# Kernel tuning notes

Hardware: AMD Instinct MI355X
Metric: run time of the kernel (lower is better)

Reference implementation:

```python
import jax, jax.numpy as jnp
import numpy as np
from jax import lax

NUM_ITER = 10
SMOOTH = 1.0
CL_WEIGHT = 0.5


def _min_pool(x, wh, ww):
    # torch: -max_pool2d(-x) pads with -inf -> min-pool with +inf boundary
    return lax.reduce_window(x, jnp.inf, lax.min,
                             (1, 1, wh, ww), (1, 1, 1, 1),
                             [(0, 0), (0, 0), (wh // 2, wh // 2), (ww // 2, ww // 2)])


def _max_pool(x, wh, ww):
    return lax.reduce_window(x, -jnp.inf, lax.max,
                             (1, 1, wh, ww), (1, 1, 1, 1),
                             [(0, 0), (0, 0), (wh // 2, wh // 2), (ww // 2, ww // 2)])


def soft_erode(img):
    return jnp.minimum(_min_pool(img, 3, 1), _min_pool(img, 1, 3))


def soft_dilate(img):
    return _max_pool(img, 3, 3)


def soft_open(img):
    return soft_dilate(soft_erode(img))


def soft_skeleton(img, num_iter=NUM_ITER):
    # img: (B,1,H,W)
    skel = jax.nn.relu(img - soft_open(img))

    def body(i, carry):
        img_e, skel = carry
        img_e = soft_erode(img_e)
        delta = jax.nn.relu(img_e - soft_open(img_e))
        skel = skel + jax.nn.relu(delta - skel * delta)
        return (img_e, skel)

    _, skel = lax.fori_loop(0, num_iter, body, (img, skel))
    return skel


def soft_dice(pred, target, smooth=SMOOTH):
    inter = jnp.sum(pred * target)
    return (2.0 * inter + smooth) / (jnp.sum(pred) + jnp.sum(target) + smooth)


def setup_inputs() -> dict:
    key = jax.random.key(0)
    k1, k2 = jax.random.split(key)
    pred = jax.random.normal(k1, (8, 1, 1024, 1024), dtype=jnp.float32)
    target = jax.random.randint(k2, (8, 1, 1024, 1024), 0, 2, dtype=jnp.int32)
    return {"pred": pred, "target": target}


def reference(pred, target):
    pred_prob = jax.nn.sigmoid(pred)          # (B,1,H,W)
    target_f = target.astype(pred_prob.dtype)

    skel_pred = soft_skeleton(pred_prob)
    skel_target = soft_skeleton(target_f)

    tprec = (jnp.sum(skel_pred * target_f) + SMOOTH) / (jnp.sum(skel_pred) + SMOOTH)
    tsens = (jnp.sum(skel_target * pred_prob) + SMOOTH) / (jnp.sum(skel_target) + SMOOTH)
    cl_dice = 2.0 * tprec * tsens / (tprec + tsens + 1e-7)

    dice = soft_dice(pred_prob, target_f)
    combined = (1.0 - CL_WEIGHT) * dice + CL_WEIGHT * cl_dice
    loss = 1.0 - combined
    return loss
```

## Files before the change

kernel.cpp:

```cpp
#include <hip/hip_runtime.h>
#include <math.h>

#define IMG  1024
#define TILE 64
#define HALO 12
#define SPP  52
#define NPRED (90*SPP)
#define SEN2 0x40004000u

typedef _Float16 h2 __attribute__((ext_vector_type(2)));
union UH { unsigned u; h2 h; };
__device__ __forceinline__ h2 u2h(unsigned u){ UH x; x.u=u; return x.h; }
__device__ __forceinline__ unsigned h2u(h2 h){ UH x; x.h=h; return x.u; }
__device__ __forceinline__ h2 pmin(h2 a, h2 b){ return __builtin_elementwise_min(a,b); }
__device__ __forceinline__ h2 pmax(h2 a, h2 b){ return __builtin_elementwise_max(a,b); }
__device__ __forceinline__ h2 funnel(h2 hi_src, h2 lo_src){
  return u2h((h2u(lo_src)>>16) | (h2u(hi_src)<<16));
}
__device__ __forceinline__ float sigmoidf(float x){ return 1.0f/(1.0f+__expf(-x)); }
__device__ __forceinline__ h2 unsent(h2 x, h2 onev, h2 zerov){
  h2 t = pmax(x-onev, zerov); return x - t - t;
}
__device__ __forceinline__ unsigned extract8(unsigned w0, unsigned w1, unsigned w2, int bp){
  unsigned long long lo = (unsigned long long)w0 | ((unsigned long long)w1<<32);
  unsigned long long hi = (unsigned long long)w1 | ((unsigned long long)w2<<32);
  unsigned a = (unsigned)(lo >> bp);
  unsigned b = (unsigned)(hi >> (bp & 31));
  return ((bp < 32) ? a : b) & 0xFFu;
}
__device__ __forceinline__ uint4 erode5(uint4 rm, uint4 rc, uint4 rn, h2 lw, h2 rv){
  h2 a0=u2h(rc.x), a1=u2h(rc.y), a2=u2h(rc.z), a3=u2h(rc.w);
  h2 v0=pmin(u2h(rm.x), u2h(rn.x));
  h2 v1=pmin(u2h(rm.y), u2h(rn.y));
  h2 v2=pmin(u2h(rm.z), u2h(rn.z));
  h2 v3=pmin(u2h(rm.w), u2h(rn.w));
  h2 f0=funnel(a0,lw), f1=funnel(a1,a0), f2=funnel(a2,a1), f3=funnel(a3,a2), f4=funnel(rv,a3);
  uint4 e;
  e.x=h2u(pmin(pmin(f0,f1),pmin(v0,a0)));
  e.y=h2u(pmin(pmin(f1,f2),pmin(v1,a1)));
  e.z=h2u(pmin(pmin(f2,f3),pmin(v2,a2)));
  e.w=h2u(pmin(pmin(f3,f4),pmin(v3,a3)));
  return e;
}

template<bool BND>
__device__ void pipeline(const float* __restrict__ pred, const int* __restrict__ targ,
                         long base, int gr0, int gc0, int tid,
                         unsigned* A, unsigned* B, unsigned* Ta, unsigned* Tb,
                         h2 val[4], h2 skel[4], unsigned &tbits, unsigned &skbits) {
  for (int i = tid; i < 104; i += 512) {
    int r = (i < 52) ? 0 : 89, c = (i < 52) ? i : i - 52;
    A[r*SPP + c] = SEN2;  B[r*SPP + c] = SEN2;
  }
  for (int i = tid; i < 704; i += 512) {
    int r = 1 + (i >> 3), w = i & 7;
    w = (w < 2) ? w : 44 + w;
    A[r*SPP + w] = SEN2;  B[r*SPP + w] = SEN2;
  }
  if (!BND) {
    #pragma unroll
    for (int k=0;k<2;++k){
      int u = tid + (k<<9);
      if (u < 968){
        int r = u/11, q = u - r*11;
        long g = base + (long)(gr0+r)*IMG + gc0 + (q<<3);
        float4 pa = *(const float4*)(pred+g);
        float4 pb = *(const float4*)(pred+g+4);
        h2 w0 = {(_Float16)sigmoidf(pa.x), (_Float16)sigmoidf(pa.y)};
        h2 w1 = {(_Float16)sigmoidf(pa.z), (_Float16)sigmoidf(pa.w)};
        h2 w2 = {(_Float16)sigmoidf(pb.x), (_Float16)sigmoidf(pb.y)};
        h2 w3 = {(_Float16)sigmoidf(pb.z), (_Float16)sigmoidf(pb.w)};
        int o = (1+r)*SPP + 2 + (q<<2);
        uint2 d0; d0.x=h2u(w0); d0.y=h2u(w1);
        uint2 d1; d1.x=h2u(w2); d1.y=h2u(w3);
        *(uint2*)&A[o]   = d0;
        *(uint2*)&A[o+2] = d1;
      }
    }
    if (tid < 264){
      int u = tid;
      int r = u/3, w = u - r*3;
      long g = base + (long)(gr0+r)*IMG + gc0 + (w<<5);
      unsigned bits = 0;
      #pragma unroll
      for (int i=0;i<8;++i){
        if (w < 2 || i < 6) {
          int4 tv = *(const int4*)(targ + g + (i<<2));
          unsigned nib = (unsigned)(tv.x!=0) | ((unsigned)(tv.y!=0)<<1)
                       | ((unsigned)(tv.z!=0)<<2) | ((unsigned)(tv.w!=0)<<3);
          bits |= nib << (i<<2);
        }
      }
      if (w==2) bits |= 0xFF000000u;
      Ta[u] = bits;
    }
  } else {
    for (int i=tid; i<88*44; i+=512){
      int r = i/44, wd = i - r*44;
      int gr = gr0 + r;
      bool rok = (unsigned)gr < (unsigned)IMG;
      int gca = gc0 + (wd<<1), gcb = gca + 1;
      _Float16 va = (_Float16)2.0f, vb = (_Float16)2.0f;
      if (rok && (unsigned)gca < (unsigned)IMG) va = (_Float16)sigmoidf(pred[base + (long)gr*IMG + gca]);
      if (rok && (unsigned)gcb < (unsigned)IMG) vb = (_Float16)sigmoidf(pred[base + (long)gr*IMG + gcb]);
      h2 w; w.x = va; w.y = vb;
      A[(1+r)*SPP + 2 + wd] = h2u(w);
    }
    for (int u=tid; u<264; u+=512){
      int r = u/3, w = u - r*3;
      int gr = gr0 + r;
      bool rok = (unsigned)gr < (unsigned)IMG;
      unsigned bits = 0;
      for (int b=0;b<32;++b){
        int c = (w<<5) + b;
        unsigned bit = 1;
        if (c < 88) {
          int gc = gc0 + c;
          if (rok && (unsigned)gc < (unsigned)IMG) bit = (unsigned)(targ[base+(long)gr*IMG+gc] != 0);
        }
        bits |= bit << b;
      }
      Ta[u] = bits;
    }
  }
  __syncthreads();

  unsigned cm0=~0u, cm1=~0u, cm2=0x00FFFFFFu;
  bool colO = false;
  if (BND) {
    int lo = (-gc0 > 0) ? -gc0 : 0;
    int hi = (IMG - gc0 < 88) ? (IMG - gc0) : 88;
    colO = (lo > 0) || (hi < 88);
    unsigned m[3];
    #pragma unroll
    for (int w=0; w<3; ++w){
      int l = lo - (w<<5); if (l<0) l=0;
      int h = hi - (w<<5); if (h>32) h=32;
      unsigned mm = 0;
      if (h > l) {
        unsigned top = (h>=32)? ~0u : ((1u<<h)-1u);
        unsigned bot = (l<=0)? 0u : ((1u<<l)-1u);
        mm = top & ~bot;
      }
      m[w]=mm;
    }
    cm0=m[0]; cm1=m[1]; cm2=m[2] & 0x00FFFFFF;
  }

  const int es  = tid / 12,  eq  = tid - es*12;
  const int s2  = es*2;
  const int ew  = eq << 2;
  const int cl1 = (eq<<3) + 3;
  const int ch1 = (eq<<3) - 4;
  const bool has2 = (tid < 16);
  const int u2  = 512 + tid;
  const int es2 = u2/12, eq2 = u2 - es2*12;
  const int s2b = es2*2, ew2 = eq2<<2;
  const int cl2 = (eq2<<3)+3, ch2 = (eq2<<3)-4;

  const bool tex = (tid < 258);
  const int  to  = 3 + tid;
  const int  twd = tid % 3;

  const int qc = tid & 7;
  const int rg = tid >> 3;
  const int pr = HALO + rg;
  const int wq = 8 + (qc<<2);
  const int bp = 12 + (qc<<3);

  h2 ep[4];
  {
    uint4 a0 = *(const uint4*)&A[(pr+1)*SPP + wq];
    ep[0]=u2h(a0.x); ep[1]=u2h(a0.y); ep[2]=u2h(a0.z); ep[3]=u2h(a0.w);
    #pragma unroll
    for (int i=0;i<4;++i){ val[i]=ep[i]; skel[i]=(h2)(_Float16)0.0f; }
  }
  {
    int oa = pr*3;
    tbits = extract8(Ta[oa],Ta[oa+1],Ta[oa+2],bp);
  }
  unsigned tp0=0,tp1=0,tp2=0, sk0=0,sk1=0,sk2=0;
  const bool td = (tid < 64);
  const int tro = (12 + tid)*3;
  if (td) { tp0=Ta[tro]; tp1=Ta[tro+1]; tp2=Ta[tro+2]; }

  const h2 onev  = {(_Float16)1.0f,(_Float16)1.0f};
  const h2 zerov = {(_Float16)0.0f,(_Float16)0.0f};

  for (int j=0;j<11;++j){
    {
      auto ERO = [&](int s2_, int ew_){
        uint4 rm = *(const uint4*)&A[s2_*SPP + ew_];
        uint4 rc = *(const uint4*)&A[(s2_+1)*SPP + ew_];
        #pragma unroll
        for (int t=0;t<2;++t){
          uint4 rn = *(const uint4*)&A[(s2_+2+t)*SPP + ew_];
          int brc = s2_+1+t;
          h2 lw = u2h(A[brc*SPP + ew_ - 1]);
          h2 rv = u2h(A[brc*SPP + ew_ + 4]);
          *(uint4*)&B[brc*SPP + ew_] = erode5(rm, rc, rn, lw, rv);
          rm = rc; rc = rn;
        }
      };
      if ((s2+1 >= j+1) && (s2 <= 86-j) && (cl1 >= j+1) && (ch1 <= 86-j))
        ERO(s2, ew);
      if (has2 && (s2b+1 >= j+1) && (s2b <= 86-j) && (cl2 >= j+1) && (ch2 <= 86-j))
        ERO(s2b, ew2);
    }
    if (tex){
      unsigned own=Ta[to], up=Ta[to-3], dn=Ta[to+3];
      unsigned le = (twd>0)? Ta[to-1] : ~0u;
      unsigned ri = (twd<2)? Ta[to+1] : ~0u;
      unsigned h = own & ((own>>1)|(ri<<31)) & ((own<<1)|(le>>31));
      Tb[to] = h & up & dn;
    }
    __syncthreads();

    if (BND) {
      if (gr0 < 0) {
        for (int i=tid;i<12*44;i+=512){ int r=i/44; B[(1+r)*SPP+2+(i-r*44)] = SEN2; }
        if (tid < 36) Tb[tid] = ~0u;
      }
      if (gr0 + 88 > IMG) {
        for (int i=tid;i<12*44;i+=512){ int r=i/44; B[(77+r)*SPP+2+(i-r*44)] = SEN2; }
        if (tid < 36) Tb[228+tid] = ~0u;
      }
      if (colO) {
        if (gc0 < 0)
          for (int i=tid;i<88*6;i+=512){ int r=i/6; B[(1+r)*SPP+2+(i-r*6)] = SEN2; }
        if (gc0 + 88 > IMG)
          for (int i=tid;i<88*6;i+=512){ int r=i/6; B[(1+r)*SPP+40+(i-r*6)] = SEN2; }
        for (int i=tid;i<264;i+=512){
          int r=i/3, w=i-r*3;
          unsigned nm = (w==0)?~cm0:((w==1)?~cm1:~cm2);
          Tb[i] |= nm;
        }
      }
      __syncthreads();
    }

    {
      h2 H[3][4];
      uint4 cap;
      #pragma unroll
      for (int k=0;k<3;++k){
        int ro = (pr+k)*SPP + wq;
        uint4 c = *(const uint4*)&B[ro];
        h2 lwv = u2h(B[ro-1]);
        h2 rwv = u2h(B[ro+4]);
        if (k==1) cap = c;
        h2 a0=u2h(c.x),a1=u2h(c.y),a2=u2h(c.z),a3=u2h(c.w);
        if (BND){
          a0=unsent(a0,onev,zerov); a1=unsent(a1,onev,zerov);
          a2=unsent(a2,onev,zerov); a3=unsent(a3,onev,zerov);
          lwv=unsent(lwv,onev,zerov); rwv=unsent(rwv,onev,zerov);
        }
        h2 f0=funnel(a0,lwv), f1=funnel(a1,a0), f2=funnel(a2,a1), f3=funnel(a3,a2), f4=funnel(rwv,a3);
        H[k][0]=pmax(pmax(f0,f1),a0);
        H[k][1]=pmax(pmax(f1,f2),a1);
        H[k][2]=pmax(pmax(f2,f3),a2);
        H[k][3]=pmax(pmax(f3,f4),a3);
      }
      #pragma unroll
      for (int i=0;i<4;++i){
        h2 m0 = pmax(pmax(H[0][i],H[1][i]),H[2][i]);
        h2 d0 = pmax(ep[i]-m0, zerov);
        h2 x0 = d0 - skel[i]*d0;
        skel[i] = skel[i] + pmax(x0, zerov);
      }
      ep[0]=u2h(cap.x); ep[1]=u2h(cap.y); ep[2]=u2h(cap.z); ep[3]=u2h(cap.w);
    }

    if (td) {
      unsigned o0=Tb[tro], o1=Tb[tro+1], o2=Tb[tro+2];
      unsigned u0=Tb[tro-3], u1=Tb[tro-2], u2v=Tb[tro-1];
      unsigned n0=Tb[tro+3], n1=Tb[tro+4], n2=Tb[tro+5];
      unsigned v0,v1,v2;
      if (BND){
        unsigned mu = ((unsigned)(gr0 + 11 + tid) < (unsigned)IMG) ? ~0u : 0u;
        unsigned md = ((unsigned)(gr0 + 13 + tid) < (unsigned)IMG) ? ~0u : 0u;
        v0 = ((u0&mu)|o0|(n0&md)) & cm0;
        v1 = ((u1&mu)|o1|(n1&md)) & cm1;
        v2 = ((u2v&mu)|o2|(n2&md)) & cm2;
      } else {
        v0 = u0|o0|n0; v1 = u1|o1|n1; v2 = u2v|o2|n2;
      }
      unsigned d0 = v0 | (v0<<1) | (v0>>1) | (v1<<31);
      unsigned d1 = v1 | (v1<<1) | (v0>>31) | (v1>>1) | (v2<<31);
      unsigned d2 = v2 | (v2<<1) | (v1>>31) | (v2>>1);
      sk0 |= tp0 & ~d0;
      sk1 |= tp1 & ~d1;
      sk2 |= tp2 & ~d2;
      tp0 = o0; tp1 = o1; tp2 = o2;
    }
    unsigned* t1 = A;  A = B;  B = t1;
    unsigned* t2 = Ta; Ta = Tb; Tb = t2;
  }

  __syncthreads();
  if (td){ Ta[3*tid]=sk0; Ta[3*tid+1]=sk1; Ta[3*tid+2]=sk2; }
  __syncthreads();
  {
    int o = rg*3;
    skbits = extract8(Ta[o],Ta[o+1],Ta[o+2],bp);
  }
}

__global__ __launch_bounds__(512,8)
void cl_dice_main(const float* __restrict__ pred, const int* __restrict__ targ,
                  float* __restrict__ ws) {
  __shared__ alignas(16) unsigned sPA[NPRED];
  __shared__ alignas(16) unsigned sPB[NPRED];
  __shared__ unsigned sTA[264], sTB[264];
  const int tid = threadIdx.x;
  const int gr0 = blockIdx.y * TILE - HALO;
  const int gc0 = blockIdx.x * TILE - HALO;
  const long base = (long)blockIdx.z * (long)(IMG * IMG);

  h2 val[4], skel[4]; unsigned tbits, skbits;
  const bool bnd = (blockIdx.x == 0) | (blockIdx.x == gridDim.x - 1) |
                   (blockIdx.y == 0) | (blockIdx.y == gridDim.y - 1);
  if (!bnd) pipeline<false>(pred, targ, base, gr0, gc0, tid, sPA, sPB, sTA, sTB, val, skel, tbits, skbits);
  else      pipeline<true >(pred, targ, base, gr0, gc0, tid, sPA, sPB, sTA, sTB, val, skel, tbits, skbits);

  float s[7] = {0,0,0,0,0,0,0};
  #pragma unroll
  for (int k=0;k<4;++k){
    int bb = k<<1;
    float p0=(float)val[k].x,  p1=(float)val[k].y;
    float a0=(float)skel[k].x, a1=(float)skel[k].y;
    float t0=(float)((tbits>>bb)&1u),  t1=(float)((tbits>>(bb+1))&1u);
    float b0=(float)((skbits>>bb)&1u), b1=(float)((skbits>>(bb+1))&1u);
    s[0]+=a0+a1;        s[1]+=a0*t0+a1*t1;
    s[2]+=b0+b1;        s[3]+=b0*p0+b1*p1;
    s[4]+=p0*t0+p1*t1;  s[5]+=p0+p1;  s[6]+=t0+t1;
  }

  float* red = (float*)sPA;
  #pragma unroll
  for (int k=0;k<7;++k){
    float v = s[k];
    v += __shfl_down(v,32); v += __shfl_down(v,16); v += __shfl_down(v,8);
    v += __shfl_down(v,4);  v += __shfl_down(v,2);  v += __shfl_down(v,1);
    if ((tid & 63) == 0) red[(tid>>6)*8 + k] = v;
  }
  __syncthreads();
  if (tid < 7) {
    float v = 0.f;
    #pragma unroll
    for (int w8=0; w8<8; ++w8) v += red[w8*8 + tid];
    int blk = (blockIdx.z * gridDim.y + blockIdx.y) * gridDim.x + blockIdx.x;
    ws[blk*8 + tid] = v;
  }
}

__global__ __launch_bounds__(256)
void cl_dice_finalize(const float* __restrict__ ws, float* __restrict__ out, int nblk) {
  __shared__ float red[4][8];
  int tid = threadIdx.x;
  float acc[7] = {0,0,0,0,0,0,0};
  for (int i=tid; i<nblk; i+=256) {
    #pragma unroll
    for (int k=0;k<7;++k) acc[k] += ws[i*8 + k];
  }
  #pragma unroll
  for (int k=0;k<7;++k){
    float v = acc[k];
    v += __shfl_down(v,32); v += __shfl_down(v,16); v += __shfl_down(v,8);
    v += __shfl_down(v,4);  v += __shfl_down(v,2);  v += __shfl_down(v,1);
    if ((tid & 63) == 0) red[tid>>6][k] = v;
  }
  __syncthreads();
  if (tid == 0) {
    float t0[7];
    #pragma unroll
    for (int k=0;k<7;++k) t0[k] = red[0][k] + red[1][k] + red[2][k] + red[3][k];
    float sum_sp = t0[0], sum_spt = t0[1], sum_st = t0[2], sum_stp = t0[3];
    float inter  = t0[4], sum_p   = t0[5], sum_t  = t0[6];
    float tprec = (sum_spt + 1.0f) / (sum_sp + 1.0f);
    float tsens = (sum_stp + 1.0f) / (sum_st + 1.0f);
    float cl    = 2.0f * tprec * tsens / (tprec + tsens + 1e-7f);
    float dice  = (2.0f * inter + 1.0f) / (sum_p + sum_t + 1.0f);
    out[0] = 1.0f - 0.5f * (dice + cl);
  }
}

extern "C" void kernel_launch(void* const* d_in, const int* in_sizes, int n_in,
                              void* d_out, int out_size, void* d_ws, size_t ws_size,
                              hipStream_t stream) {
  const float* pred = (const float*)d_in[0];
  const int*   targ = (const int*)d_in[1];
  float* ws  = (float*)d_ws;
  float* out = (float*)d_out;

  const int B = in_sizes[0] / (IMG * IMG);
  dim3 grid(IMG / TILE, IMG / TILE, B);
  cl_dice_main<<<grid, 512, 0, stream>>>(pred, targ, ws);

  const int nblk = (IMG / TILE) * (IMG / TILE) * B;
  cl_dice_finalize<<<1, 256, 0, stream>>>(ws, out, nblk);
}
```

Baseline: 251.9 us.

## Rewrite skeleton kernel as register-resident per-wavefront column strips with DPP shifts

Replaces the shared-memory tiled pipeline with a design where each wavefront owns a 64-column strip (40 output columns plus halo). Each lane keeps 88 rows of packed fp16 values and target bitmasks in registers, and horizontal neighbours are fetched with DPP row shifts. This removes the LDS traffic and the per-iteration __syncthreads. The cost is very high register pressure (cur/nxt/val/skel arrays at occupancy 1), redundant halo loads that are uncoalesced scalar per-lane reads, and a DPP row_shr/shl neighbour exchange whose reach across 16-lane rows needs checking.

```diff
diff --git a/kernel.cpp b/kernel.cpp
--- a/kernel.cpp
+++ b/kernel.cpp
@@ -1,356 +1,176 @@
 #include <hip/hip_runtime.h>
 #include <math.h>
 
-#define IMG  1024
-#define TILE 64
-#define HALO 12
-#define SPP  52
-#define NPRED (90*SPP)
-#define SEN2 0x40004000u
+#define IMG 1024
+#define NXT 26
+#define NYT 16
+#define WPB 4
 
 typedef _Float16 h2 __attribute__((ext_vector_type(2)));
 union UH { unsigned u; h2 h; };
 __device__ __forceinline__ h2 u2h(unsigned u){ UH x; x.u=u; return x.h; }
 __device__ __forceinline__ unsigned h2u(h2 h){ UH x; x.h=h; return x.u; }
-__device__ __forceinline__ h2 pmin(h2 a, h2 b){ return __builtin_elementwise_min(a,b); }
-__device__ __forceinline__ h2 pmax(h2 a, h2 b){ return __builtin_elementwise_max(a,b); }
-__device__ __forceinline__ h2 funnel(h2 hi_src, h2 lo_src){
-  return u2h((h2u(lo_src)>>16) | (h2u(hi_src)<<16));
+__device__ __forceinline__ h2 pmin(h2 a,h2 b){ return __builtin_elementwise_min(a,b); }
+__device__ __forceinline__ h2 pmax(h2 a,h2 b){ return __builtin_elementwise_max(a,b); }
+__device__ __forceinline__ h2 funnel(h2 hi_src,h2 lo_src){ return u2h((h2u(lo_src)>>16)|(h2u(hi_src)<<16)); }
+__device__ __forceinline__ unsigned wshr(unsigned old_,unsigned src){
+  return (unsigned)__builtin_amdgcn_update_dpp((int)old_,(int)src,0x138,0xF,0xF,false);
+}
+__device__ __forceinline__ unsigned wshl(unsigned old_,unsigned src){
+  return (unsigned)__builtin_amdgcn_update_dpp((int)old_,(int)src,0x130,0xF,0xF,false);
 }
 __device__ __forceinline__ float sigmoidf(float x){ return 1.0f/(1.0f+__expf(-x)); }
-__device__ __forceinline__ h2 unsent(h2 x, h2 onev, h2 zerov){
-  h2 t = pmax(x-onev, zerov); return x - t - t;
-}
-__device__ __forceinline__ unsigned extract8(unsigned w0, unsigned w1, unsigned w2, int bp){
-  unsigned long long lo = (unsigned long long)w0 | ((unsigned long long)w1<<32);
-  unsigned long long hi = (unsigned long long)w1 | ((unsigned long long)w2<<32);
-  unsigned a = (unsigned)(lo >> bp);
-  unsigned b = (unsigned)(hi >> (bp & 31));
-  return ((bp < 32) ? a : b) & 0xFFu;
-}
-__device__ __forceinline__ uint4 erode5(uint4 rm, uint4 rc, uint4 rn, h2 lw, h2 rv){
-  h2 a0=u2h(rc.x), a1=u2h(rc.y), a2=u2h(rc.z), a3=u2h(rc.w);
-  h2 v0=pmin(u2h(rm.x), u2h(rn.x));
-  h2 v1=pmin(u2h(rm.y), u2h(rn.y));
-  h2 v2=pmin(u2h(rm.z), u2h(rn.z));
-  h2 v3=pmin(u2h(rm.w), u2h(rn.w));
-  h2 f0=funnel(a0,lw), f1=funnel(a1,a0), f2=funnel(a2,a1), f3=funnel(a3,a2), f4=funnel(rv,a3);
-  uint4 e;
-  e.x=h2u(pmin(pmin(f0,f1),pmin(v0,a0)));
-  e.y=h2u(pmin(pmin(f1,f2),pmin(v1,a1)));
-  e.z=h2u(pmin(pmin(f2,f3),pmin(v2,a2)));
-  e.w=h2u(pmin(pmin(f3,f4),pmin(v3,a3)));
-  return e;
-}
-
-template<bool BND>
-__device__ void pipeline(const float* __restrict__ pred, const int* __restrict__ targ,
-                         long base, int gr0, int gc0, int tid,
-                         unsigned* A, unsigned* B, unsigned* Ta, unsigned* Tb,
-                         h2 val[4], h2 skel[4], unsigned &tbits, unsigned &skbits) {
-  for (int i = tid; i < 104; i += 512) {
-    int r = (i < 52) ? 0 : 89, c = (i < 52) ? i : i - 52;
-    A[r*SPP + c] = SEN2;  B[r*SPP + c] = SEN2;
-  }
-  for (int i = tid; i < 704; i += 512) {
-    int r = 1 + (i >> 3), w = i & 7;
-    w = (w < 2) ? w : 44 + w;
-    A[r*SPP + w] = SEN2;  B[r*SPP + w] = SEN2;
-  }
-  if (!BND) {
-    #pragma unroll
-    for (int k=0;k<2;++k){
-      int u = tid + (k<<9);
-      if (u < 968){
-        int r = u/11, q = u - r*11;
-        long g = base + (long)(gr0+r)*IMG + gc0 + (q<<3);
-        float4 pa = *(const float4*)(pred+g);
-        float4 pb = *(const float4*)(pred+g+4);
-        h2 w0 = {(_Float16)sigmoidf(pa.x), (_Float16)sigmoidf(pa.y)};
-        h2 w1 = {(_Float16)sigmoidf(pa.z), (_Float16)sigmoidf(pa.w)};
-        h2 w2 = {(_Float16)sigmoidf(pb.x), (_Float16)sigmoidf(pb.y)};
-        h2 w3 = {(_Float16)sigmoidf(pb.z), (_Float16)sigmoidf(pb.w)};
-        int o = (1+r)*SPP + 2 + (q<<2);
-        uint2 d0; d0.x=h2u(w0); d0.y=h2u(w1);
-        uint2 d1; d1.x=h2u(w2); d1.y=h2u(w3);
-        *(uint2*)&A[o]   = d0;
-        *(uint2*)&A[o+2] = d1;
-      }
-    }
-    if (tid < 264){
-      int u = tid;
-      int r = u/3, w = u - r*3;
-      long g = base + (long)(gr0+r)*IMG + gc0 + (w<<5);
-      unsigned bits = 0;
-      #pragma unroll
-      for (int i=0;i<8;++i){
-        if (w < 2 || i < 6) {
-          int4 tv = *(const int4*)(targ + g + (i<<2));
-          unsigned nib = (unsigned)(tv.x!=0) | ((unsigned)(tv.y!=0)<<1)
-                       | ((unsigned)(tv.z!=0)<<2) | ((unsigned)(tv.w!=0)<<3);
-          bits |= nib << (i<<2);
-        }
-      }
-      if (w==2) bits |= 0xFF000000u;
-      Ta[u] = bits;
-    }
-  } else {
-    for (int i=tid; i<88*44; i+=512){
-      int r = i/44, wd = i - r*44;
-      int gr = gr0 + r;
-      bool rok = (unsigned)gr < (unsigned)IMG;
-      int gca = gc0 + (wd<<1), gcb = gca + 1;
-      _Float16 va = (_Float16)2.0f, vb = (_Float16)2.0f;
-      if (rok && (unsigned)gca < (unsigned)IMG) va = (_Float16)sigmoidf(pred[base + (long)gr*IMG + gca]);
-      if (rok && (unsigned)gcb < (unsigned)IMG) vb = (_Float16)sigmoidf(pred[base + (long)gr*IMG + gcb]);
-      h2 w; w.x = va; w.y = vb;
-      A[(1+r)*SPP + 2 + wd] = h2u(w);
-    }
-    for (int u=tid; u<264; u+=512){
-      int r = u/3, w = u - r*3;
-      int gr = gr0 + r;
-      bool rok = (unsigned)gr < (unsigned)IMG;
-      unsigned bits = 0;
-      for (int b=0;b<32;++b){
-        int c = (w<<5) + b;
-        unsigned bit = 1;
-        if (c < 88) {
-          int gc = gc0 + c;
-          if (rok && (unsigned)gc < (unsigned)IMG) bit = (unsigned)(targ[base+(long)gr*IMG+gc] != 0);
-        }
-        bits |= bit << b;
-      }
-      Ta[u] = bits;
-    }
-  }
-  __syncthreads();
-
-  unsigned cm0=~0u, cm1=~0u, cm2=0x00FFFFFFu;
-  bool colO = false;
-  if (BND) {
-    int lo = (-gc0 > 0) ? -gc0 : 0;
-    int hi = (IMG - gc0 < 88) ? (IMG - gc0) : 88;
-    colO = (lo > 0) || (hi < 88);
+
+__global__ __launch_bounds__(256,1)
+void cl_dice_main(const float* __restrict__ pred, const int* __restrict__ targ,
+                  float* __restrict__ ws){
+  __shared__ float red[WPB][8];
+  const int tid  = threadIdx.x;
+  const int lane = tid & 63, wv = tid >> 6;
+  const int wid  = blockIdx.x*WPB + wv;
+  const int tx   = wid % NXT; const int tt = wid / NXT;
+  const int ty   = tt % NYT;  const int z  = tt / NYT;
+  const long base = (long)z*IMG*IMG;
+  const int or0 = ty*64 - 12;
+  const int oc0 = tx*40;
+  const int c   = oc0 - 12 + lane;
+  const bool cv = (unsigned)c < (unsigned)IMG;
+  const int cc  = (c<0)?0:((c>IMG-1)?IMG-1:c);
+  const int lo  = (or0<0)? -or0 : 0;
+  const int hi  = (IMG-or0 < 88)? (IMG-or0) : 88;
+
+  unsigned rm0,rm1,rm2;
+  {
     unsigned m[3];
     #pragma unroll
-    for (int w=0; w<3; ++w){
-      int l = lo - (w<<5); if (l<0) l=0;
-      int h = hi - (w<<5); if (h>32) h=32;
-      unsigned mm = 0;
-      if (h > l) {
-        unsigned top = (h>=32)? ~0u : ((1u<<h)-1u);
-        unsigned bot = (l<=0)? 0u : ((1u<<l)-1u);
-        mm = top & ~bot;
-      }
+    for (int w=0;w<3;++w){
+      int l = lo-32*w; l = l<0?0:(l>32?32:l);
+      int h = hi-32*w; h = h<0?0:(h>32?32:h);
+      unsigned mm=0;
+      if (h>l){ unsigned top=(h>=32)?~0u:((1u<<h)-1u); unsigned bot=(l<=0)?0u:((1u<<l)-1u); mm=top&~bot; }
       m[w]=mm;
     }
-    cm0=m[0]; cm1=m[1]; cm2=m[2] & 0x00FFFFFF;
-  }
-
-  const int es  = tid / 12,  eq  = tid - es*12;
-  const int s2  = es*2;
-  const int ew  = eq << 2;
-  const int cl1 = (eq<<3) + 3;
-  const int ch1 = (eq<<3) - 4;
-  const bool has2 = (tid < 16);
-  const int u2  = 512 + tid;
-  const int es2 = u2/12, eq2 = u2 - es2*12;
-  const int s2b = es2*2, ew2 = eq2<<2;
-  const int cl2 = (eq2<<3)+3, ch2 = (eq2<<3)-4;
-
-  const bool tex = (tid < 258);
-  const int  to  = 3 + tid;
-  const int  twd = tid % 3;
-
-  const int qc = tid & 7;
-  const int rg = tid >> 3;
-  const int pr = HALO + rg;
-  const int wq = 8 + (qc<<2);
-  const int bp = 12 + (qc<<3);
-
-  h2 ep[4];
-  {
-    uint4 a0 = *(const uint4*)&A[(pr+1)*SPP + wq];
-    ep[0]=u2h(a0.x); ep[1]=u2h(a0.y); ep[2]=u2h(a0.z); ep[3]=u2h(a0.w);
-    #pragma unroll
-    for (int i=0;i<4;++i){ val[i]=ep[i]; skel[i]=(h2)(_Float16)0.0f; }
-  }
-  {
-    int oa = pr*3;
-    tbits = extract8(Ta[oa],Ta[oa+1],Ta[oa+2],bp);
-  }
-  unsigned tp0=0,tp1=0,tp2=0, sk0=0,sk1=0,sk2=0;
-  const bool td = (tid < 64);
-  const int tro = (12 + tid)*3;
-  if (td) { tp0=Ta[tro]; tp1=Ta[tro+1]; tp2=Ta[tro+2]; }
-
-  const h2 onev  = {(_Float16)1.0f,(_Float16)1.0f};
-  const h2 zerov = {(_Float16)0.0f,(_Float16)0.0f};
-
+    rm0=m[0]; rm1=m[1]; rm2=m[2];
+  }
+  const unsigned cinv = cv ? 0u : ~0u;
+  const unsigned nr0 = ~rm0 | cinv, nr1 = ~rm1 | cinv, nr2 = ~rm2 | cinv;
+  const unsigned pm0 = rm0 & ~cinv, pm1 = rm1 & ~cinv, pm2 = rm2 & ~cinv;
+
+  const h2 twos  = { (_Float16)2.0f, (_Float16)2.0f };
+  const h2 zerov = { (_Float16)0.0f, (_Float16)0.0f };
+
+  h2 cur[44]; unsigned t0=0,t1=0,t2=0xFF000000u;
+  const float* pb = pred + base;
+  const int*   tb = targ + base;
+  #pragma unroll
+  for (int k=0;k<44;++k){
+    int r0 = or0 + 2*k, r1 = r0 + 1;
+    int g0 = r0<0?0:(r0>IMG-1?IMG-1:r0);
+    int g1 = r1<0?0:(r1>IMG-1?IMG-1:r1);
+    float x0 = pb[(long)g0*IMG + cc];
+    float x1 = pb[(long)g1*IMG + cc];
+    int   v0 = tb[(long)g0*IMG + cc];
+    int   v1 = tb[(long)g1*IMG + cc];
+    h2 hh; hh.x=(_Float16)sigmoidf(x0); hh.y=(_Float16)sigmoidf(x1);
+    cur[k]=hh;
+    unsigned add = ((unsigned)(v0!=0) << ((2*k)&31)) | ((unsigned)(v1!=0) << ((2*k+1)&31));
+    if (k<16) t0|=add; else if (k<32) t1|=add; else t2|=add;
+  }
+  h2 val[32];
+  #pragma unroll
+  for (int i=0;i<32;++i) val[i]=cur[i+6];
+  const unsigned q0=t0,q1=t1,q2=t2;
+  unsigned sk0=0,sk1=0,sk2=0;
+  h2 skel[32];
+  #pragma unroll
+  for (int i=0;i<32;++i) skel[i]=zerov;
+
+  h2 nxt[44];
   for (int j=0;j<11;++j){
-    {
-      auto ERO = [&](int s2_, int ew_){
-        uint4 rm = *(const uint4*)&A[s2_*SPP + ew_];
-        uint4 rc = *(const uint4*)&A[(s2_+1)*SPP + ew_];
-        #pragma unroll
-        for (int t=0;t<2;++t){
-          uint4 rn = *(const uint4*)&A[(s2_+2+t)*SPP + ew_];
-          int brc = s2_+1+t;
-          h2 lw = u2h(A[brc*SPP + ew_ - 1]);
-          h2 rv = u2h(A[brc*SPP + ew_ + 4]);
-          *(uint4*)&B[brc*SPP + ew_] = erode5(rm, rc, rn, lw, rv);
-          rm = rc; rc = rn;
-        }
-      };
-      if ((s2+1 >= j+1) && (s2 <= 86-j) && (cl1 >= j+1) && (ch1 <= 86-j))
-        ERO(s2, ew);
-      if (has2 && (s2b+1 >= j+1) && (s2b <= 86-j) && (cl2 >= j+1) && (ch2 <= 86-j))
-        ERO(s2b, ew2);
+    h2 mm = twos;
+    h2 mc;
+    { h2 x=cur[0]; x = cv ? x : twos; if (0 < lo) x = twos; mc = x; }
+    #pragma unroll
+    for (int k=0;k<44;++k){
+      h2 mn;
+      if (k<43){
+        h2 x = cur[k+1];
+        x = cv ? x : twos;
+        if (2*(k+1) < lo || 2*(k+1) >= hi) x = twos;
+        mn = x;
+      } else mn = twos;
+      h2 su = funnel(mc, mm);
+      h2 sd = funnel(mn, mc);
+      h2 v3 = pmin(pmin(su,sd), mc);
+      h2 l3 = u2h(wshr(h2u(twos), h2u(mc)));
+      h2 r3 = u2h(wshl(h2u(twos), h2u(mc)));
+      h2 h3 = pmin(pmin(l3,r3), mc);
+      nxt[k] = pmin(v3,h3);
+      mm = mc; mc = mn;
     }
-    if (tex){
-      unsigned own=Ta[to], up=Ta[to-3], dn=Ta[to+3];
-      unsigned le = (twd>0)? Ta[to-1] : ~0u;
-      unsigned ri = (twd<2)? Ta[to+1] : ~0u;
-      unsigned h = own & ((own>>1)|(ri<<31)) & ((own<<1)|(le>>31));
-      Tb[to] = h & up & dn;
+    unsigned e0 = t0|nr0, e1 = t1|nr1, e2 = t2|nr2;
+    unsigned U0 = (e0<<1)|1u,        U1=(e1<<1)|(e0>>31), U2=(e2<<1)|(e1>>31);
+    unsigned D0 = (e0>>1)|(e1<<31),  D1=(e1>>1)|(e2<<31), D2=(e2>>1)|0x80000000u;
+    unsigned L0 = wshr(~0u,e0), L1 = wshr(~0u,e1), L2 = wshr(~0u,e2);
+    unsigned R0 = wshl(~0u,e0), R1 = wshl(~0u,e1), R2 = wshl(~0u,e2);
+    unsigned n0 = e0&U0&D0&L0&R0, n1 = e1&U1&D1&L1&R1, n2 = e2&U2&D2&L2&R2;
+    unsigned g0 = n0&pm0, g1 = n1&pm1, g2 = n2&pm2;
+    unsigned V0 = g0|(g0<<1)|((g0>>1)|(g1<<31));
+    unsigned V1 = g1|((g1<<1)|(g0>>31))|((g1>>1)|(g2<<31));
+    unsigned V2 = g2|((g2<<1)|(g1>>31))|(g2>>1);
+    unsigned d0 = V0|wshr(0u,V0)|wshl(0u,V0);
+    unsigned d1 = V1|wshr(0u,V1)|wshl(0u,V1);
+    unsigned d2 = V2|wshr(0u,V2)|wshl(0u,V2);
+    sk0 |= t0&~d0; sk1 |= t1&~d1; sk2 |= t2&~d2;
+    t0=n0; t1=n1; t2=n2;
+    h2 dm, dc;
+    { h2 x=nxt[5]; x = cv ? x : zerov; if (10 < lo || 10 >= hi) x = zerov; dm = x; }
+    { h2 x=nxt[6]; x = cv ? x : zerov; if (12 < lo || 12 >= hi) x = zerov; dc = x; }
+    #pragma unroll
+    for (int k=6;k<38;++k){
+      h2 dn;
+      { h2 x = nxt[k+1]; x = cv ? x : zerov;
+        if (2*(k+1) < lo || 2*(k+1) >= hi) x = zerov; dn = x; }
+      h2 vm = pmax(pmax(funnel(dc,dm), funnel(dn,dc)), dc);
+      h2 lm = u2h(wshr(0u, h2u(vm)));
+      h2 rr = u2h(wshl(0u, h2u(vm)));
+      h2 hm = pmax(pmax(lm,rr), vm);
+      h2 d  = pmax(cur[k]-hm, zerov);
+      h2 x2 = d - skel[k-6]*d;
+      skel[k-6] = skel[k-6] + pmax(x2, zerov);
+      dm = dc; dc = dn;
     }
-    __syncthreads();
-
-    if (BND) {
-      if (gr0 < 0) {
-        for (int i=tid;i<12*44;i+=512){ int r=i/44; B[(1+r)*SPP+2+(i-r*44)] = SEN2; }
-        if (tid < 36) Tb[tid] = ~0u;
-      }
-      if (gr0 + 88 > IMG) {
-        for (int i=tid;i<12*44;i+=512){ int r=i/44; B[(77+r)*SPP+2+(i-r*44)] = SEN2; }
-        if (tid < 36) Tb[228+tid] = ~0u;
-      }
-      if (colO) {
-        if (gc0 < 0)
-          for (int i=tid;i<88*6;i+=512){ int r=i/6; B[(1+r)*SPP+2+(i-r*6)] = SEN2; }
-        if (gc0 + 88 > IMG)
-          for (int i=tid;i<88*6;i+=512){ int r=i/6; B[(1+r)*SPP+40+(i-r*6)] = SEN2; }
-        for (int i=tid;i<264;i+=512){
-          int r=i/3, w=i-r*3;
-          unsigned nm = (w==0)?~cm0:((w==1)?~cm1:~cm2);
-          Tb[i] |= nm;
-        }
-      }
-      __syncthreads();
-    }
-
-    {
-      h2 H[3][4];
-      uint4 cap;
-      #pragma unroll
-      for (int k=0;k<3;++k){
-        int ro = (pr+k)*SPP + wq;
-        uint4 c = *(const uint4*)&B[ro];
-        h2 lwv = u2h(B[ro-1]);
-        h2 rwv = u2h(B[ro+4]);
-        if (k==1) cap = c;
-        h2 a0=u2h(c.x),a1=u2h(c.y),a2=u2h(c.z),a3=u2h(c.w);
-        if (BND){
-          a0=unsent(a0,onev,zerov); a1=unsent(a1,onev,zerov);
-          a2=unsent(a2,onev,zerov); a3=unsent(a3,onev,zerov);
-          lwv=unsent(lwv,onev,zerov); rwv=unsent(rwv,onev,zerov);
-        }
-        h2 f0=funnel(a0,lwv), f1=funnel(a1,a0), f2=funnel(a2,a1), f3=funnel(a3,a2), f4=funnel(rwv,a3);
-        H[k][0]=pmax(pmax(f0,f1),a0);
-        H[k][1]=pmax(pmax(f1,f2),a1);
-        H[k][2]=pmax(pmax(f2,f3),a2);
-        H[k][3]=pmax(pmax(f3,f4),a3);
-      }
-      #pragma unroll
-      for (int i=0;i<4;++i){
-        h2 m0 = pmax(pmax(H[0][i],H[1][i]),H[2][i]);
-        h2 d0 = pmax(ep[i]-m0, zerov);
-        h2 x0 = d0 - skel[i]*d0;
-        skel[i] = skel[i] + pmax(x0, zerov);
-      }
-      ep[0]=u2h(cap.x); ep[1]=u2h(cap.y); ep[2]=u2h(cap.z); ep[3]=u2h(cap.w);
-    }
-
-    if (td) {
-      unsigned o0=Tb[tro], o1=Tb[tro+1], o2=Tb[tro+2];
-      unsigned u0=Tb[tro-3], u1=Tb[tro-2], u2v=Tb[tro-1];
-      unsigned n0=Tb[tro+3], n1=Tb[tro+4], n2=Tb[tro+5];
-      unsigned v0,v1,v2;
-      if (BND){
-        unsigned mu = ((unsigned)(gr0 + 11 + tid) < (unsigned)IMG) ? ~0u : 0u;
-        unsigned md = ((unsigned)(gr0 + 13 + tid) < (unsigned)IMG) ? ~0u : 0u;
-        v0 = ((u0&mu)|o0|(n0&md)) & cm0;
-        v1 = ((u1&mu)|o1|(n1&md)) & cm1;
-        v2 = ((u2v&mu)|o2|(n2&md)) & cm2;
-      } else {
-        v0 = u0|o0|n0; v1 = u1|o1|n1; v2 = u2v|o2|n2;
-      }
-      unsigned d0 = v0 | (v0<<1) | (v0>>1) | (v1<<31);
-      unsigned d1 = v1 | (v1<<1) | (v0>>31) | (v1>>1) | (v2<<31);
-      unsigned d2 = v2 | (v2<<1) | (v1>>31) | (v2>>1);
-      sk0 |= tp0 & ~d0;
-      sk1 |= tp1 & ~d1;
-      sk2 |= tp2 & ~d2;
-      tp0 = o0; tp1 = o1; tp2 = o2;
-    }
-    unsigned* t1 = A;  A = B;  B = t1;
-    unsigned* t2 = Ta; Ta = Tb; Tb = t2;
-  }
-
-  __syncthreads();
-  if (td){ Ta[3*tid]=sk0; Ta[3*tid+1]=sk1; Ta[3*tid+2]=sk2; }
-  __syncthreads();
-  {
-    int o = rg*3;
-    skbits = extract8(Ta[o],Ta[o+1],Ta[o+2],bp);
-  }
-}
-
-__global__ __launch_bounds__(512,8)
-void cl_dice_main(const float* __restrict__ pred, const int* __restrict__ targ,
-                  float* __restrict__ ws) {
-  __shared__ alignas(16) unsigned sPA[NPRED];
-  __shared__ alignas(16) unsigned sPB[NPRED];
-  __shared__ unsigned sTA[264], sTB[264];
-  const int tid = threadIdx.x;
-  const int gr0 = blockIdx.y * TILE - HALO;
-  const int gc0 = blockIdx.x * TILE - HALO;
-  const long base = (long)blockIdx.z * (long)(IMG * IMG);
-
-  h2 val[4], skel[4]; unsigned tbits, skbits;
-  const bool bnd = (blockIdx.x == 0) | (blockIdx.x == gridDim.x - 1) |
-                   (blockIdx.y == 0) | (blockIdx.y == gridDim.y - 1);
-  if (!bnd) pipeline<false>(pred, targ, base, gr0, gc0, tid, sPA, sPB, sTA, sTB, val, skel, tbits, skbits);
-  else      pipeline<true >(pred, targ, base, gr0, gc0, tid, sPA, sPB, sTA, sTB, val, skel, tbits, skbits);
-
-  float s[7] = {0,0,0,0,0,0,0};
-  #pragma unroll
-  for (int k=0;k<4;++k){
-    int bb = k<<1;
-    float p0=(float)val[k].x,  p1=(float)val[k].y;
-    float a0=(float)skel[k].x, a1=(float)skel[k].y;
-    float t0=(float)((tbits>>bb)&1u),  t1=(float)((tbits>>(bb+1))&1u);
-    float b0=(float)((skbits>>bb)&1u), b1=(float)((skbits>>(bb+1))&1u);
-    s[0]+=a0+a1;        s[1]+=a0*t0+a1*t1;
-    s[2]+=b0+b1;        s[3]+=b0*p0+b1*p1;
-    s[4]+=p0*t0+p1*t1;  s[5]+=p0+p1;  s[6]+=t0+t1;
-  }
-
-  float* red = (float*)sPA;
+    #pragma unroll
+    for (int k=0;k<44;++k) cur[k]=nxt[k];
+  }
+
+  float s[7]={0,0,0,0,0,0,0};
+  #pragma unroll
+  for (int i=0;i<32;++i){
+    const int k=i+6;
+    const int b=(2*k)&31;
+    const int w=(2*k)>>5;
+    unsigned qw = (w==0)?q0:((w==1)?q1:q2);
+    unsigned sw = (w==0)?sk0:((w==1)?sk1:sk2);
+    float p0=(float)val[i].x,  p1=(float)val[i].y;
+    float a0=(float)skel[i].x, a1=(float)skel[i].y;
+    float tb0=(float)((qw>>b)&1u), tb1=(float)((qw>>(b+1))&1u);
+    float sb0=(float)((sw>>b)&1u), sb1=(float)((sw>>(b+1))&1u);
+    s[0]+=a0+a1;          s[1]+=a0*tb0+a1*tb1;
+    s[2]+=sb0+sb1;        s[3]+=sb0*p0+sb1*p1;
+    s[4]+=p0*tb0+p1*tb1;  s[5]+=p0+p1;  s[6]+=tb0+tb1;
+  }
+  const float msk = ((lane>=12)&&(lane<=51)&&(c<IMG)) ? 1.0f : 0.0f;
   #pragma unroll
   for (int k=0;k<7;++k){
-    float v = s[k];
+    float v = s[k]*msk;
     v += __shfl_down(v,32); v += __shfl_down(v,16); v += __shfl_down(v,8);
     v += __shfl_down(v,4);  v += __shfl_down(v,2);  v += __shfl_down(v,1);
-    if ((tid & 63) == 0) red[(tid>>6)*8 + k] = v;
+    if (lane==0) red[wv][k]=v;
   }
   __syncthreads();
-  if (tid < 7) {
-    float v = 0.f;
-    #pragma unroll
-    for (int w8=0; w8<8; ++w8) v += red[w8*8 + tid];
-    int blk = (blockIdx.z * gridDim.y + blockIdx.y) * gridDim.x + blockIdx.x;
-    ws[blk*8 + tid] = v;
+  if (tid<7){
+    ws[blockIdx.x*8+tid] = red[0][tid]+red[1][tid]+red[2][tid]+red[3][tid];
   }
 }
 
@@ -394,9 +214,8 @@
   float* out = (float*)d_out;
 
   const int B = in_sizes[0] / (IMG * IMG);
-  dim3 grid(IMG / TILE, IMG / TILE, B);
-  cl_dice_main<<<grid, 512, 0, stream>>>(pred, targ, ws);
-
-  const int nblk = (IMG / TILE) * (IMG / TILE) * B;
+  const int nw   = NXT*NYT*B;
+  const int nblk = nw / WPB;
+  cl_dice_main<<<nblk, 256, 0, stream>>>(pred, targ, ws);
   cl_dice_finalize<<<1, 256, 0, stream>>>(ws, out, nblk);
 }
```

Measured after the change: 272.0 us. +8.0%, slower.
